# Performance work log

Measured on AMD Instinct MI355X. Metric: run time of the kernel, lower is better.

Reference implementation:

```python
import jax, jax.numpy as jnp
import numpy as np

K_SIZE, STRIDE, PAD = 3, 1, 1
B, C1, C2, H, W = 2, 256, 256, 64, 64


def conv2d(x, w, b, stride, pad):
    out = jax.lax.conv_general_dilated(
        x, w, (stride, stride), [(pad, pad), (pad, pad)],
        dimension_numbers=("NCHW", "OIHW", "NCHW"))
    return out + b[None, :, None, None]


def deform_conv2d(x, offset, mask, w, b, k, stride, pad):
    # torchvision.ops.deform_conv2d semantics (modulated, offset_groups=1)
    Bn, C, Hh, Ww = x.shape
    Ho, Wo = offset.shape[2], offset.shape[3]
    K = k * k
    # offset channels are (dy, dx) interleaved per kernel point
    off = offset.reshape(Bn, K, 2, Ho, Wo)
    dy, dx = off[:, :, 0], off[:, :, 1]          # [B,K,Ho,Wo]
    ki = jnp.arange(k)
    kyy, kxx = jnp.meshgrid(ki, ki, indexing="ij")
    kyy, kxx = kyy.reshape(K), kxx.reshape(K)
    base_y = (jnp.arange(Ho) * stride - pad)[None, :, None] + kyy[:, None, None]  # [K,Ho,1]
    base_x = (jnp.arange(Wo) * stride - pad)[None, None, :] + kxx[:, None, None]  # [K,1,Wo]
    ys = base_y[None].astype(x.dtype) + dy       # [B,K,Ho,Wo]
    xs = base_x[None].astype(x.dtype) + dx
    N = K * Ho * Wo
    ysf, xsf = ys.reshape(Bn, N), xs.reshape(Bn, N)
    y0 = jnp.floor(ysf)
    x0 = jnp.floor(xsf)
    ly, lx = ysf - y0, xsf - x0                  # bilinear fractions
    y0i, x0i = y0.astype(jnp.int32), x0.astype(jnp.int32)
    xf = x.reshape(Bn, C, Hh * Ww)

    def gather(yi, xi):
        valid = (yi >= 0) & (yi < Hh) & (xi >= 0) & (xi < Ww)
        idx = jnp.clip(yi, 0, Hh - 1) * Ww + jnp.clip(xi, 0, Ww - 1)
        v = jnp.take_along_axis(xf, idx[:, None, :], axis=2)  # [B,C,N]
        return v * valid[:, None, :].astype(x.dtype)

    v00 = gather(y0i, x0i)
    v01 = gather(y0i, x0i + 1)
    v10 = gather(y0i + 1, x0i)
    v11 = gather(y0i + 1, x0i + 1)
    wy1, wx1 = ly[:, None], lx[:, None]
    val = (v00 * (1 - wy1) * (1 - wx1) + v01 * (1 - wy1) * wx1 +
           v10 * wy1 * (1 - wx1) + v11 * wy1 * wx1)          # [B,C,N]
    val = val.reshape(Bn, C, K, Ho, Wo) * mask[:, None]       # modulate
    out = jnp.einsum("ock,bckhw->bohw", w.reshape(w.shape[0], C, K), val)
    return out + b[None, :, None, None]


def setup_inputs() -> dict:
    key = jax.random.key(0)
    ks = jax.random.split(key, 6)
    k2 = K_SIZE * K_SIZE
    return {
        "x": jax.random.normal(ks[0], (B, C1, H, W), jnp.float32),
        "offset_feat": jax.random.normal(ks[1], (B, C2, H, W), jnp.float32),
        # offset/mask head conv (zero-init in module; small random so offsets are non-trivial)
        "w_offset_mask": jax.random.normal(ks[2], (3 * k2, C2, K_SIZE, K_SIZE), jnp.float32) * 0.01,
        "b_offset_mask": jax.random.normal(ks[3], (3 * k2,), jnp.float32) * 0.01,
        "w_dcn": jax.random.normal(ks[4], (C2, C1, K_SIZE, K_SIZE), jnp.float32) / np.sqrt(C1 * k2),
        "b_dcn": jax.random.normal(ks[5], (C2,), jnp.float32) * 0.01,
    }


def reference(x, offset_feat, w_offset_mask, b_offset_mask, w_dcn, b_dcn):
    om = conv2d(offset_feat, w_offset_mask, b_offset_mask, STRIDE, PAD)  # [B,3*k*k,Ho,Wo]
    o1, o2, m = jnp.split(om, 3, axis=1)
    offset = jnp.concatenate([o1, o2], axis=1)   # [B,2*k*k,Ho,Wo]
    mask = jax.nn.sigmoid(m)                      # [B,k*k,Ho,Wo]
    return deform_conv2d(x, offset, mask, w_dcn, b_dcn, K_SIZE, STRIDE, PAD)
```

## Files before the change

kernel.cpp:

```cpp
#include <hip/hip_runtime.h>
#include <math.h>

#define BATCH 2
#define CIN   256
#define COUT  256
#define COFF  256
#define HWPIX 4096
#define CKTOT 2304
#define VSTR  40
#define PH    66
#define PHW   4356

typedef __attribute__((ext_vector_type(8))) short short8;
typedef __attribute__((ext_vector_type(8))) unsigned short ushort8;
typedef __attribute__((ext_vector_type(4))) float float4v;

__device__ __forceinline__ unsigned short f2bf(float f) {
    unsigned u = __float_as_uint(f);
    unsigned r = (u + 0x7FFFu + ((u >> 16) & 1u)) >> 16;
    return (unsigned short)r;
}
__device__ __forceinline__ float bf2f(unsigned short h) {
    return __uint_as_float(((unsigned)h) << 16);
}

__global__ __launch_bounds__(256) void prep_kernel(
    const float* __restrict__ x, const float* __restrict__ feat,
    const float* __restrict__ wdcn, const float* __restrict__ wom,
    unsigned short* __restrict__ xTh,
    unsigned short* __restrict__ fh,
    unsigned short* __restrict__ whi,
    unsigned short* __restrict__ wohi,
    float* __restrict__ out)
{
    const int bid = blockIdx.x;
    const int tid = threadIdx.x;

    if (bid < 4096) {
        const bool isx = bid < 2048;
        const int lb = isx ? bid : bid - 2048;
        const int b  = lb >> 10;
        const int r  = lb & 1023;
        const int pt = r >> 3;
        const int ct = r & 7;
        __shared__ float t[32][33];
        const int tx = tid & 31, ty = tid >> 5;
        const float* src = isx ? x : feat;
        const float* sb = src + ((size_t)b * 256 + ct * 32) * HWPIX + pt * 32;
#pragma unroll
        for (int i = ty; i < 32; i += 8)
            t[i][tx] = sb[(size_t)i * HWPIX + tx];
        __syncthreads();
        if (isx) {
            unsigned short* ob = xTh + ((size_t)b * HWPIX + pt * 32) * 256 + ct * 32;
#pragma unroll
            for (int i = ty; i < 32; i += 8)
                ob[(size_t)i * 256 + tx] = f2bf(t[tx][i]);
        } else {
#pragma unroll
            for (int i = ty; i < 32; i += 8) {
                int p = pt * 32 + i;
                int row = (p >> 6) + 1, col = (p & 63) + 1;
                fh[((size_t)b * PHW + row * PH + col) * 256 + ct * 32 + tx]
                    = f2bf(t[tx][i]);
            }
        }
    } else if (bid < 6400) {
        int gid = (bid - 4096) * 256 + tid;
        int cc  = gid & 31;
        int co  = (gid >> 5) & 255;
        int kcb = gid >> 13;
        int k   = kcb >> 3;
        int cb  = kcb & 7;
        float w = wdcn[((size_t)co * 256 + cb * 32 + cc) * 9 + k];
        whi[gid] = f2bf(w);
    } else if (bid < 6688) {
        int gid = (bid - 6400) * 256 + tid;
        int cc  = gid & 31;
        int co  = (gid >> 5) & 31;
        int kcb = gid >> 10;
        int k   = kcb >> 3;
        int cb  = kcb & 7;
        float w = 0.0f;
        if (co < 27) w = wom[(size_t)co * CKTOT + (cb * 32 + cc) * 9 + k];
        wohi[gid] = f2bf(w);
    } else if (bid < 7208) {
        int idx = (bid - 6688) * 256 + tid;
        int b = idx / 66560;
        int r = idx - b * 66560;
        int pidx = r >> 8;
        int c = r & 255;
        int row, col;
        if (pidx < 66)       { row = 0;           col = pidx; }
        else if (pidx < 132) { row = 65;          col = pidx - 66; }
        else if (pidx < 196) { row = pidx - 131;  col = 0; }
        else                 { row = pidx - 195;  col = 65; }
        fh[((size_t)b * PHW + row * PH + col) * 256 + c] = 0;
    } else {
        int idx = (bid - 7208) * 256 + tid;
        ((float4*)out)[idx] = make_float4(0.f, 0.f, 0.f, 0.f);
    }
}

__global__ __launch_bounds__(256) void conv_om_fused_kernel(
    const unsigned short* __restrict__ fh,
    const unsigned short* __restrict__ wohi,
    const float* __restrict__ bom,
    float4* __restrict__ wt4,
    int4*   __restrict__ ix4)
{
    const int tile = blockIdx.x;
    const int b    = blockIdx.y;
    const int y    = tile >> 2;
    const int xb   = (tile & 3) * 16;
    const int tid  = threadIdx.x;
    const int wv   = tid >> 6;
    const int lane = tid & 63;
    const int l15  = lane & 15;
    const int q    = lane >> 4;

    __shared__ float red[4][32][16];

    float4v acc[2];
    acc[0] = (float4v)0.0f;
    acc[1] = (float4v)0.0f;

    const unsigned short* fhb = fh + (size_t)b * PHW * 256;

#pragma unroll 6
    for (int i = 0; i < 18; ++i) {
        int kcb = wv * 18 + i;
        int k  = kcb >> 3;
        int cb = kcb & 7;
        size_t s = ((size_t)((y + k / 3) * PH + xb + l15 + k % 3)) * 256 + cb * 32 + q * 8;
        short8 bh  = *(const short8*)(fhb + s);
        short8 ah0 = *(const short8*)(wohi + ((size_t)kcb * 32 + l15) * 32 + q * 8);
        short8 ah1 = *(const short8*)(wohi + ((size_t)kcb * 32 + 16 + l15) * 32 + q * 8);
        acc[0] = __builtin_amdgcn_mfma_f32_16x16x32_bf16(ah0, bh, acc[0], 0, 0, 0);
        acc[1] = __builtin_amdgcn_mfma_f32_16x16x32_bf16(ah1, bh, acc[1], 0, 0, 0);
    }

#pragma unroll
    for (int t = 0; t < 2; ++t)
#pragma unroll
        for (int r = 0; r < 4; ++r)
            red[wv][t * 16 + q * 4 + r][l15] = acc[t][r];
    __syncthreads();

    if (tid < 144) {
        int k   = tid >> 4;
        int pxl = tid & 15;
        float dy = bom[2 * k]     + red[0][2 * k][pxl]     + red[1][2 * k][pxl]
                                  + red[2][2 * k][pxl]     + red[3][2 * k][pxl];
        float dx = bom[2 * k + 1] + red[0][2 * k + 1][pxl] + red[1][2 * k + 1][pxl]
                                  + red[2][2 * k + 1][pxl] + red[3][2 * k + 1][pxl];
        float mm = bom[18 + k]    + red[0][18 + k][pxl]    + red[1][18 + k][pxl]
                                  + red[2][18 + k][pxl]    + red[3][18 + k][pxl];
        int xx = xb + pxl;
        float ys = (float)(y  - 1 + (k / 3)) + dy;
        float xs = (float)(xx - 1 + (k % 3)) + dx;
        float y0f = floorf(ys), x0f = floorf(xs);
        int y0 = (int)y0f, x0 = (int)x0f;
        float ly = ys - y0f, lx = xs - x0f;
        float m  = 1.0f / (1.0f + expf(-mm));
        bool yv0 = ((unsigned)y0 < 64u), yv1 = ((unsigned)(y0 + 1) < 64u);
        bool xv0 = ((unsigned)x0 < 64u), xv1 = ((unsigned)(x0 + 1) < 64u);
        int i00 = (y0 * 64 + x0) << 8;
        float4 wt;
        int4 ix;
        wt.x = (yv0 && xv0) ? (1.0f - ly) * (1.0f - lx) * m : 0.0f;
        wt.y = (yv0 && xv1) ? (1.0f - ly) * lx * m          : 0.0f;
        wt.z = (yv1 && xv0) ? ly * (1.0f - lx) * m          : 0.0f;
        wt.w = (yv1 && xv1) ? ly * lx * m                   : 0.0f;
        ix.x = (yv0 && xv0) ? i00          : 0;
        ix.y = (yv0 && xv1) ? i00 + 256    : 0;
        ix.z = (yv1 && xv0) ? i00 + 16384  : 0;
        ix.w = (yv1 && xv1) ? i00 + 16640  : 0;
        int dst = ((b * 9 + k) << 12) + y * 64 + xx;
        wt4[dst] = wt;
        ix4[dst] = ix;
    }
}

__global__ __launch_bounds__(512, 4) void dcn_mfma_kernel(
    const unsigned short* __restrict__ xTh,
    const float4* __restrict__ wt4,
    const int4* __restrict__ ix4,
    const unsigned short* __restrict__ whi,
    const float* __restrict__ bdcn,
    float* __restrict__ out)
{
    const int tid = threadIdx.x;
    const int y   = blockIdx.x >> 1;
    const int xh  = blockIdx.x & 1;
    const int kg  = blockIdx.y;
    const int b   = blockIdx.z;

    __shared__ float4 s_wt[288];
    __shared__ int4   s_ix[288];
    __shared__ unsigned short V[288 * VSTR];

    if (tid < 288) {
        int k   = tid >> 5;
        int pxl = tid & 31;
        int p   = y * 64 + xh * 32 + pxl;
        int src = ((b * 9 + k) << 12) + p;
        s_wt[tid] = wt4[src];
        s_ix[tid] = ix4[src];
    }
    __syncthreads();

    const int w    = tid >> 6;
    const int lane = tid & 63;
    const int l15  = lane & 15;
    const int q    = lane >> 4;

    const int cg   = tid & 3;
    const int spx  = (tid >> 2) & 31;
    const int tapg = tid >> 7;

    float4v acc[2][2];
#pragma unroll
    for (int t = 0; t < 2; ++t)
#pragma unroll
        for (int p = 0; p < 2; ++p) acc[t][p] = (float4v)0.0f;

    const unsigned short* xb = xTh + ((size_t)b << 12) * 256;

    for (int cbl = 0; cbl < 4; ++cbl) {
        const int cb = kg * 4 + cbl;

        {
            const unsigned short* xc = xb + cb * 32 + cg * 8;
#pragma unroll 3
            for (int j = 0; j < 3; ++j) {
                int k = tapg + 4 * j;
                if (k > 8) break;
                int cidx = k * 32 + spx;
                float4 wt = s_wt[cidx];
                int4   ix = s_ix[cidx];
                ushort8 u00 = *(const ushort8*)(xc + ix.x);
                ushort8 u01 = *(const ushort8*)(xc + ix.y);
                ushort8 u10 = *(const ushort8*)(xc + ix.z);
                ushort8 u11 = *(const ushort8*)(xc + ix.w);
                unsigned hv[4];
#pragma unroll
                for (int jj = 0; jj < 4; ++jj) {
                    float va = wt.x * bf2f(u00[2 * jj])     + wt.y * bf2f(u01[2 * jj])
                             + wt.z * bf2f(u10[2 * jj])     + wt.w * bf2f(u11[2 * jj]);
                    float vb = wt.x * bf2f(u00[2 * jj + 1]) + wt.y * bf2f(u01[2 * jj + 1])
                             + wt.z * bf2f(u10[2 * jj + 1]) + wt.w * bf2f(u11[2 * jj + 1]);
                    hv[jj] = (unsigned)f2bf(va) | ((unsigned)f2bf(vb) << 16);
                }
                *(uint4*)&V[cidx * VSTR + cg * 8]
                    = make_uint4(hv[0], hv[1], hv[2], hv[3]);
            }
        }
        __syncthreads();

#pragma unroll 3
        for (int k = 0; k < 9; ++k) {
            const int kcb = k * 8 + cb;
            size_t base = ((size_t)kcb * 256 + w * 32 + l15) * 32 + q * 8;
            short8 ah0 = *(const short8*)(whi + base);
            short8 ah1 = *(const short8*)(whi + base + 16 * 32);
            short8 bh0 = *(const short8*)&V[(k * 32 + l15) * VSTR + q * 8];
            short8 bh1 = *(const short8*)&V[(k * 32 + 16 + l15) * VSTR + q * 8];
            acc[0][0] = __builtin_amdgcn_mfma_f32_16x16x32_bf16(ah0, bh0, acc[0][0], 0, 0, 0);
            acc[0][1] = __builtin_amdgcn_mfma_f32_16x16x32_bf16(ah0, bh1, acc[0][1], 0, 0, 0);
            acc[1][0] = __builtin_amdgcn_mfma_f32_16x16x32_bf16(ah1, bh0, acc[1][0], 0, 0, 0);
            acc[1][1] = __builtin_amdgcn_mfma_f32_16x16x32_bf16(ah1, bh1, acc[1][1], 0, 0, 0);
        }
        __syncthreads();
    }

#pragma unroll
    for (int t = 0; t < 2; ++t) {
#pragma unroll
        for (int r = 0; r < 4; ++r) {
            int co = w * 32 + t * 16 + q * 4 + r;
            float bias = (kg == 0) ? bdcn[co] : 0.0f;
#pragma unroll
            for (int p = 0; p < 2; ++p) {
                int px = xh * 32 + p * 16 + l15;
                atomicAdd(&out[(((size_t)b * COUT + co) << 12) + y * 64 + px],
                          acc[t][p][r] + bias);
            }
        }
    }
}

extern "C" void kernel_launch(void* const* d_in, const int* in_sizes, int n_in,
                              void* d_out, int out_size, void* d_ws, size_t ws_size,
                              hipStream_t stream)
{
    const float* x    = (const float*)d_in[0];
    const float* feat = (const float*)d_in[1];
    const float* wom  = (const float*)d_in[2];
    const float* bom  = (const float*)d_in[3];
    const float* wdcn = (const float*)d_in[4];
    const float* bdcn = (const float*)d_in[5];
    float* out = (float*)d_out;

    unsigned short* whi  = (unsigned short*)d_ws;
    unsigned short* wohi = whi + (size_t)CKTOT * 256;
    unsigned short* xTh  = wohi + 73728;
    unsigned short* fh   = xTh + (size_t)2 * HWPIX * 256;
    float4* wt4          = (float4*)(fh + (size_t)2 * PHW * 256);
    int4*   ix4          = (int4*)(wt4 + (size_t)2 * 9 * HWPIX);

    prep_kernel<<<9256, 256, 0, stream>>>(x, feat, wdcn, wom, xTh, fh,
                                          whi, wohi, out);

    dim3 gom(256, 2);
    conv_om_fused_kernel<<<gom, 256, 0, stream>>>(fh, wohi, bom, wt4, ix4);

    dim3 grid(128, 2, 2);
    dcn_mfma_kernel<<<grid, 512, 0, stream>>>(xTh, wt4, ix4, whi, bdcn, out);
}
```

Before: 127.7 us.

## Fuse offset/mask conv into DCN kernel and drop split-K atomics

```diff
diff --git a/kernel.cpp b/kernel.cpp
--- a/kernel.cpp
+++ b/kernel.cpp
@@ -30,8 +30,7 @@
     unsigned short* __restrict__ xTh,
     unsigned short* __restrict__ fh,
     unsigned short* __restrict__ whi,
-    unsigned short* __restrict__ wohi,
-    float* __restrict__ out)
+    unsigned short* __restrict__ wohi)
 {
     const int bid = blockIdx.x;
     const int tid = threadIdx.x;
@@ -84,7 +83,7 @@
         float w = 0.0f;
         if (co < 27) w = wom[(size_t)co * CKTOT + (cb * 32 + cc) * 9 + k];
         wohi[gid] = f2bf(w);
-    } else if (bid < 7208) {
+    } else {
         int idx = (bid - 6688) * 256 + tid;
         int b = idx / 66560;
         int r = idx - b * 66560;
@@ -96,67 +95,78 @@
         else if (pidx < 196) { row = pidx - 131;  col = 0; }
         else                 { row = pidx - 195;  col = 65; }
         fh[((size_t)b * PHW + row * PH + col) * 256 + c] = 0;
-    } else {
-        int idx = (bid - 7208) * 256 + tid;
-        ((float4*)out)[idx] = make_float4(0.f, 0.f, 0.f, 0.f);
-    }
-}
-
-__global__ __launch_bounds__(256) void conv_om_fused_kernel(
+    }
+}
+
+__global__ __launch_bounds__(512, 4) void dcn_fused_kernel(
+    const unsigned short* __restrict__ xTh,
     const unsigned short* __restrict__ fh,
+    const unsigned short* __restrict__ whi,
     const unsigned short* __restrict__ wohi,
     const float* __restrict__ bom,
-    float4* __restrict__ wt4,
-    int4*   __restrict__ ix4)
+    const float* __restrict__ bdcn,
+    float* __restrict__ out)
 {
-    const int tile = blockIdx.x;
-    const int b    = blockIdx.y;
-    const int y    = tile >> 2;
-    const int xb   = (tile & 3) * 16;
-    const int tid  = threadIdx.x;
+    const int tid = threadIdx.x;
+    const int y   = blockIdx.x >> 1;
+    const int xh  = blockIdx.x & 1;
+    const int b   = blockIdx.y;
+
+    __shared__ float red[8][32][32];
+    __shared__ float4 s_wt[288];
+    __shared__ int4   s_ix[288];
+    __shared__ unsigned short V[288 * VSTR];
+
     const int wv   = tid >> 6;
     const int lane = tid & 63;
     const int l15  = lane & 15;
     const int q    = lane >> 4;
 
-    __shared__ float red[4][32][16];
-
-    float4v acc[2];
-    acc[0] = (float4v)0.0f;
-    acc[1] = (float4v)0.0f;
-
-    const unsigned short* fhb = fh + (size_t)b * PHW * 256;
-
-#pragma unroll 6
-    for (int i = 0; i < 18; ++i) {
-        int kcb = wv * 18 + i;
-        int k  = kcb >> 3;
-        int cb = kcb & 7;
-        size_t s = ((size_t)((y + k / 3) * PH + xb + l15 + k % 3)) * 256 + cb * 32 + q * 8;
-        short8 bh  = *(const short8*)(fhb + s);
-        short8 ah0 = *(const short8*)(wohi + ((size_t)kcb * 32 + l15) * 32 + q * 8);
-        short8 ah1 = *(const short8*)(wohi + ((size_t)kcb * 32 + 16 + l15) * 32 + q * 8);
-        acc[0] = __builtin_amdgcn_mfma_f32_16x16x32_bf16(ah0, bh, acc[0], 0, 0, 0);
-        acc[1] = __builtin_amdgcn_mfma_f32_16x16x32_bf16(ah1, bh, acc[1], 0, 0, 0);
-    }
-
-#pragma unroll
-    for (int t = 0; t < 2; ++t)
-#pragma unroll
-        for (int r = 0; r < 4; ++r)
-            red[wv][t * 16 + q * 4 + r][l15] = acc[t][r];
+    {
+        float4v aco[2][2];
+#pragma unroll
+        for (int t = 0; t < 2; ++t)
+#pragma unroll
+            for (int p = 0; p < 2; ++p) aco[t][p] = (float4v)0.0f;
+
+        const unsigned short* fhb = fh + (size_t)b * PHW * 256;
+#pragma unroll 3
+        for (int i = 0; i < 9; ++i) {
+            int kcb = wv * 9 + i;
+            int k  = kcb >> 3;
+            int cb = kcb & 7;
+            size_t s = ((size_t)((y + k / 3) * PH + xh * 32 + (k % 3))) * 256
+                     + cb * 32 + q * 8;
+            short8 bh0 = *(const short8*)(fhb + s + (size_t)l15 * 256);
+            short8 bh1 = *(const short8*)(fhb + s + (size_t)(16 + l15) * 256);
+            short8 ah0 = *(const short8*)(wohi + ((size_t)kcb * 32 + l15) * 32 + q * 8);
+            short8 ah1 = *(const short8*)(wohi + ((size_t)kcb * 32 + 16 + l15) * 32 + q * 8);
+            aco[0][0] = __builtin_amdgcn_mfma_f32_16x16x32_bf16(ah0, bh0, aco[0][0], 0, 0, 0);
+            aco[0][1] = __builtin_amdgcn_mfma_f32_16x16x32_bf16(ah0, bh1, aco[0][1], 0, 0, 0);
+            aco[1][0] = __builtin_amdgcn_mfma_f32_16x16x32_bf16(ah1, bh0, aco[1][0], 0, 0, 0);
+            aco[1][1] = __builtin_amdgcn_mfma_f32_16x16x32_bf16(ah1, bh1, aco[1][1], 0, 0, 0);
+        }
+#pragma unroll
+        for (int t = 0; t < 2; ++t)
+#pragma unroll
+            for (int p = 0; p < 2; ++p)
+#pragma unroll
+                for (int r = 0; r < 4; ++r)
+                    red[wv][t * 16 + q * 4 + r][p * 16 + l15] = aco[t][p][r];
+    }
     __syncthreads();
 
-    if (tid < 144) {
-        int k   = tid >> 4;
-        int pxl = tid & 15;
-        float dy = bom[2 * k]     + red[0][2 * k][pxl]     + red[1][2 * k][pxl]
-                                  + red[2][2 * k][pxl]     + red[3][2 * k][pxl];
-        float dx = bom[2 * k + 1] + red[0][2 * k + 1][pxl] + red[1][2 * k + 1][pxl]
-                                  + red[2][2 * k + 1][pxl] + red[3][2 * k + 1][pxl];
-        float mm = bom[18 + k]    + red[0][18 + k][pxl]    + red[1][18 + k][pxl]
-                                  + red[2][18 + k][pxl]    + red[3][18 + k][pxl];
-        int xx = xb + pxl;
+    if (tid < 288) {
+        int k   = tid >> 5;
+        int pxl = tid & 31;
+        float dy = bom[2 * k], dx = bom[2 * k + 1], mm = bom[18 + k];
+#pragma unroll
+        for (int g = 0; g < 8; ++g) {
+            dy += red[g][2 * k][pxl];
+            dx += red[g][2 * k + 1][pxl];
+            mm += red[g][18 + k][pxl];
+        }
+        int xx = xh * 32 + pxl;
         float ys = (float)(y  - 1 + (k / 3)) + dy;
         float xs = (float)(xx - 1 + (k % 3)) + dx;
         float y0f = floorf(ys), x0f = floorf(xs);
@@ -176,44 +186,12 @@
         ix.y = (yv0 && xv1) ? i00 + 256    : 0;
         ix.z = (yv1 && xv0) ? i00 + 16384  : 0;
         ix.w = (yv1 && xv1) ? i00 + 16640  : 0;
-        int dst = ((b * 9 + k) << 12) + y * 64 + xx;
-        wt4[dst] = wt;
-        ix4[dst] = ix;
-    }
-}
-
-__global__ __launch_bounds__(512, 4) void dcn_mfma_kernel(
-    const unsigned short* __restrict__ xTh,
-    const float4* __restrict__ wt4,
-    const int4* __restrict__ ix4,
-    const unsigned short* __restrict__ whi,
-    const float* __restrict__ bdcn,
-    float* __restrict__ out)
-{
-    const int tid = threadIdx.x;
-    const int y   = blockIdx.x >> 1;
-    const int xh  = blockIdx.x & 1;
-    const int kg  = blockIdx.y;
-    const int b   = blockIdx.z;
-
-    __shared__ float4 s_wt[288];
-    __shared__ int4   s_ix[288];
-    __shared__ unsigned short V[288 * VSTR];
-
-    if (tid < 288) {
-        int k   = tid >> 5;
-        int pxl = tid & 31;
-        int p   = y * 64 + xh * 32 + pxl;
-        int src = ((b * 9 + k) << 12) + p;
-        s_wt[tid] = wt4[src];
-        s_ix[tid] = ix4[src];
+        s_wt[tid] = wt;
+        s_ix[tid] = ix;
     }
     __syncthreads();
 
-    const int w    = tid >> 6;
-    const int lane = tid & 63;
-    const int l15  = lane & 15;
-    const int q    = lane >> 4;
+    const int w = tid >> 6;
 
     const int cg   = tid & 3;
     const int spx  = (tid >> 2) & 31;
@@ -227,9 +205,7 @@
 
     const unsigned short* xb = xTh + ((size_t)b << 12) * 256;
 
-    for (int cbl = 0; cbl < 4; ++cbl) {
-        const int cb = kg * 4 + cbl;
-
+    for (int cb = 0; cb < 8; ++cb) {
         {
             const unsigned short* xc = xb + cb * 32 + cg * 8;
 #pragma unroll 3
@@ -279,12 +255,12 @@
 #pragma unroll
         for (int r = 0; r < 4; ++r) {
             int co = w * 32 + t * 16 + q * 4 + r;
-            float bias = (kg == 0) ? bdcn[co] : 0.0f;
+            float bias = bdcn[co];
 #pragma unroll
             for (int p = 0; p < 2; ++p) {
                 int px = xh * 32 + p * 16 + l15;
-                atomicAdd(&out[(((size_t)b * COUT + co) << 12) + y * 64 + px],
-                          acc[t][p][r] + bias);
+                out[(((size_t)b * COUT + co) << 12) + y * 64 + px]
+                    = acc[t][p][r] + bias;
             }
         }
     }
@@ -306,15 +282,11 @@
     unsigned short* wohi = whi + (size_t)CKTOT * 256;
     unsigned short* xTh  = wohi + 73728;
     unsigned short* fh   = xTh + (size_t)2 * HWPIX * 256;
-    float4* wt4          = (float4*)(fh + (size_t)2 * PHW * 256);
-    int4*   ix4          = (int4*)(wt4 + (size_t)2 * 9 * HWPIX);
-
-    prep_kernel<<<9256, 256, 0, stream>>>(x, feat, wdcn, wom, xTh, fh,
-                                          whi, wohi, out);
-
-    dim3 gom(256, 2);
-    conv_om_fused_kernel<<<gom, 256, 0, stream>>>(fh, wohi, bom, wt4, ix4);
-
-    dim3 grid(128, 2, 2);
-    dcn_mfma_kernel<<<grid, 512, 0, stream>>>(xTh, wt4, ix4, whi, bdcn, out);
-}
+
+    prep_kernel<<<7208, 256, 0, stream>>>(x, feat, wdcn, wom, xTh, fh,
+                                          whi, wohi);
+
+    dim3 grid(128, 2);
+    dcn_fused_kernel<<<grid, 512, 0, stream>>>(xTh, fh, whi, wohi,
+                                               bom, bdcn, out);
+}
```

Result: faster. 125.0 us (-2.1%).
